# Optimization experiments

Hardware: AMD Instinct MI355X
Metric: run time of the kernel (lower is better)

The kernel has to match this reference:

```python
import jax, jax.numpy as jnp
import numpy as np

H = 256      # hidden_dim
NH = 8       # num_heads
D = H // NH  # per-head dim
NEG = -(2.0**32) + 1.0
EPS = 1e-5


def setup_inputs() -> dict:
    key = jax.random.key(0)
    ks = jax.random.split(key, 12)
    N, Tq, Tk = 2, 2048, 2048
    s = 1.0 / np.sqrt(H)
    return {
        "Q": jax.random.normal(ks[0], (N, Tq, H), jnp.float32),
        "K": jax.random.normal(ks[1], (N, Tk, H), jnp.float32),
        "V": jax.random.normal(ks[2], (N, Tk, H), jnp.float32),
        "Wq": jax.random.normal(ks[3], (H, H), jnp.float32) * s,
        "bq": jnp.zeros((H,), jnp.float32),
        "Wk": jax.random.normal(ks[4], (H, H), jnp.float32) * s,
        "bk": jnp.zeros((H,), jnp.float32),
        "Wv": jax.random.normal(ks[5], (H, H), jnp.float32) * s,
        "bv": jnp.zeros((H,), jnp.float32),
        "gamma": jnp.ones((H,), jnp.float32),
        "beta": jnp.zeros((H,), jnp.float32),
    }


def _split_heads(x):
    # [N,T,H] -> [h,N,T,D]  (matches torch split(dim=2)+cat(dim=0): head-major)
    N, T, _ = x.shape
    return x.reshape(N, T, NH, D).transpose(2, 0, 1, 3)


def reference(Q, K, V, Wq, bq, Wk, bk, Wv, bv, gamma, beta):
    N, Tq, _ = Q.shape
    Tk = K.shape[1]
    Ql = jax.nn.relu(Q @ Wq + bq)
    Kl = jax.nn.relu(K @ Wk + bk)
    Vl = jax.nn.relu(V @ Wv + bv)
    Qh, Kh, Vh = _split_heads(Ql), _split_heads(Kl), _split_heads(Vl)

    scores = jnp.einsum("hnqd,hnkd->hnqk", Qh, Kh) / jnp.sqrt(jnp.float32(D))
    key_mask = jnp.sign(jnp.abs(K).sum(-1))    # [N,Tk]
    scores = jnp.where(key_mask[None, :, None, :] == 0, NEG, scores)
    attn = jax.nn.softmax(scores / 0.01, axis=-1)
    query_mask = jnp.sign(jnp.abs(Q).sum(-1))  # [N,Tq]
    attn = attn * query_mask[None, :, :, None]  # dropout p=0 -> identity

    ctx = jnp.einsum("hnqk,hnkd->hnqd", attn[..., :-1], Vh[:, :, :-1, :])
    out = ctx.transpose(1, 2, 0, 3).reshape(N, Tq, H)

    mu = out.mean(-1, keepdims=True)
    var = ((out - mu) ** 2).mean(-1, keepdims=True)
    out = (out - mu) / jnp.sqrt(var + EPS) * gamma + beta

    weight = attn.transpose(1, 2, 0, 3).reshape(N, Tq, NH * Tk).mean(-1)
    return out, weight
```

## Files before the change

### kernel.cpp

```cpp
#include <hip/hip_runtime.h>
#include <math.h>

#define H_DIM 256
#define NHEAD 8
#define DHEAD 32
#define NB 2
#define TSEQ 2048
#define LN_EPS 1e-5f

#define QK2_SCALE 25.503486f
#define SPLIT 2
#define TILES_PER (TSEQ / 64 / SPLIT)

typedef _Float16 half8 __attribute__((ext_vector_type(8)));
typedef _Float16 half4t __attribute__((ext_vector_type(4)));
typedef _Float16 half2t __attribute__((ext_vector_type(2)));
typedef float f32x4 __attribute__((ext_vector_type(4)));

__device__ __forceinline__ f32x4 mfma16(half8 a, half8 b, f32x4 c) {
  return __builtin_amdgcn_mfma_f32_16x16x32_f16(a, b, c, 0, 0, 0);
}
__device__ __forceinline__ float exp2fast(float x) {
  return __builtin_amdgcn_exp2f(x);
}
__device__ __forceinline__ half2t pkrtz(float a, float b) {
  return __builtin_bit_cast(half2t, __builtin_amdgcn_cvt_pkrtz(a, b));
}

__global__ __launch_bounds__(256) void pack_mask_kernel(
    const float* __restrict__ K,
    const float* __restrict__ Wq, const float* __restrict__ Wk, const float* __restrict__ Wv,
    float* __restrict__ kmask,
    half8* __restrict__ WpkHi, half8* __restrict__ WpkLo) {
  const int tid = threadIdx.x;
  if (blockIdx.x < 1024) {
    const int wid = tid >> 6, lane = tid & 63;
    int row = blockIdx.x * 4 + wid;
    const float* src = K + (size_t)row * H_DIM;
    float4 v = *(const float4*)(src + lane * 4);
    float s = fabsf(v.x) + fabsf(v.y) + fabsf(v.z) + fabsf(v.w);
    #pragma unroll
    for (int off = 32; off > 0; off >>= 1) s += __shfl_xor(s, off);
    if (lane == 0) kmask[row] = (s != 0.0f) ? 1.0f : 0.0f;
    return;
  }
  int slot = (blockIdx.x - 1024) * 256 + tid;
  int lane = slot & 63;
  int fg = (slot >> 6) & 15;
  int s  = (slot >> 10) & 7;
  int which = slot >> 13;
  const float* W = which == 0 ? Wq : which == 1 ? Wk : Wv;
  int j  = fg * 16 + (lane & 15);
  int kb = s * 32 + (lane >> 4) * 8;
  half8 hi, lo;
  #pragma unroll
  for (int jj = 0; jj < 8; ++jj) {
    float x = W[(size_t)(kb + jj) * H_DIM + j];
    _Float16 h = (_Float16)x;
    hi[jj] = h;
    lo[jj] = (_Float16)(x - (float)h);
  }
  WpkHi[slot] = hi;
  WpkLo[slot] = lo;
}

__global__ __launch_bounds__(256) void proj_kernel(
    const float* __restrict__ Q, const float* __restrict__ K, const float* __restrict__ V,
    const float* __restrict__ bq, const float* __restrict__ bk, const float* __restrict__ bv,
    const half8* __restrict__ WpkHi, const half8* __restrict__ WpkLo,
    const float* __restrict__ kmask,
    half8* __restrict__ Gqhi, half8* __restrict__ Gqlo,
    half8* __restrict__ Gkhi, half8* __restrict__ Gklo, half8* __restrict__ Gv,
    half8* __restrict__ AmaskF, float* __restrict__ qmask) {
  const int which = blockIdx.z;
  const float* X    = which == 0 ? Q  : which == 1 ? K  : V;
  const float* bias = which == 0 ? bq : which == 1 ? bk : bv;

  __shared__ __align__(16) float T[64 * 68];

  const int tid = threadIdx.x;
  const int w = tid >> 6, lane = tid & 63;
  const int l15 = lane & 15, quad = lane >> 4;
  const int mbase = blockIdx.y * 64;
  const int nfg   = blockIdx.x * 4;
  const int nn   = mbase >> 11;
  const int tile = blockIdx.y & 31;

  half8 ahi[8], alo[8];
  {
    const bool doqm = (which == 0) && (blockIdx.x == 0);
    float sabs = 0.0f;
    const float* xrow = X + (size_t)(mbase + w * 16 + l15) * H_DIM + quad * 8;
    #pragma unroll
    for (int s = 0; s < 8; ++s) {
      float4 a0 = *(const float4*)(xrow + s * 32);
      float4 a1 = *(const float4*)(xrow + s * 32 + 4);
      float xs[8] = {a0.x, a0.y, a0.z, a0.w, a1.x, a1.y, a1.z, a1.w};
      if (doqm) {
        #pragma unroll
        for (int i = 0; i < 8; ++i) sabs += fabsf(xs[i]);
      }
      #pragma unroll
      for (int i = 0; i < 8; ++i) {
        _Float16 h = (_Float16)xs[i];
        ahi[s][i] = h;
        alo[s][i] = (_Float16)(xs[i] - (float)h);
      }
    }
    if (doqm) {
      sabs += __shfl_xor(sabs, 16);
      sabs += __shfl_xor(sabs, 32);
      if (quad == 0) qmask[mbase + w * 16 + l15] = (sabs != 0.0f) ? 1.0f : 0.0f;
    }
  }

  f32x4 acc[4];
  #pragma unroll
  for (int f = 0; f < 4; ++f) acc[f] = (f32x4){0.f, 0.f, 0.f, 0.f};

  #pragma unroll
  for (int s = 0; s < 8; ++s) {
    const half8* ph = WpkHi + (((size_t)which * 8 + s) * 16 + nfg) * 64 + lane;
    const half8* pl = WpkLo + (((size_t)which * 8 + s) * 16 + nfg) * 64 + lane;
    #pragma unroll
    for (int f = 0; f < 4; ++f) {
      half8 BH = ph[f * 64];
      half8 BL = pl[f * 64];
      acc[f] = mfma16(ahi[s], BH, acc[f]);
      acc[f] = mfma16(ahi[s], BL, acc[f]);
      acc[f] = mfma16(alo[s], BH, acc[f]);
    }
  }

  #pragma unroll
  for (int f = 0; f < 4; ++f) {
    float bj = bias[blockIdx.x * 64 + f * 16 + l15];
    #pragma unroll
    for (int r = 0; r < 4; ++r) {
      int row = w * 16 + quad * 4 + r;
      float val = fmaxf(acc[f][r] + bj, 0.0f);
      if (which == 2 && ((mbase + row) & (TSEQ - 1)) == TSEQ - 1) val = 0.0f;
      T[row * 68 + f * 16 + l15] = val;
    }
  }
  __syncthreads();

  if (which < 2) {
    const int fq = tid >> 6, lp = tid & 63;
    const int kdc = lp >> 4, krlo = lp & 15;
    const int row = fq * 16 + krlo;
    const float sc = (which == 0) ? QK2_SCALE : 1.0f;
    #pragma unroll
    for (int hs = 0; hs < 2; ++hs) {
      const float* p = &T[row * 68 + hs * 32 + kdc * 8];
      float4 a0 = *(const float4*)p;
      float4 a1 = *(const float4*)(p + 4);
      float xs[8] = {a0.x, a0.y, a0.z, a0.w, a1.x, a1.y, a1.z, a1.w};
      half8 hi, lo;
      #pragma unroll
      for (int i = 0; i < 8; ++i) {
        float x = xs[i] * sc;
        _Float16 h = (_Float16)x;
        hi[i] = h;
        lo[i] = (_Float16)(x - (float)h);
      }
      int hn = (blockIdx.x * 2 + hs) * NB + nn;
      size_t di = ((size_t)hn * 32 + tile) * 256 + tid;
      if (which == 0) { Gqhi[di] = hi; Gqlo[di] = lo; }
      else            { Gkhi[di] = hi; Gklo[di] = lo; }
    }
    if (which == 1 && blockIdx.x == 0 && tid < 128) {
      int c = tid >> 6, lane2 = tid & 63;
      int quad2 = lane2 >> 4, l15b = lane2 & 15;
      half8 am;
      #pragma unroll
      for (int j = 0; j < 8; ++j)
        am[j] = (l15b == 0) ? (_Float16)kmask[(size_t)nn * TSEQ + tile * 64 + c * 32 + quad2 * 8 + j]
                            : (_Float16)0.0f;
      AmaskF[(((size_t)nn * 32 + tile) * 2 + c) * 64 + lane2] = am;
    }
  } else {
    const int top = tid >> 6, mid = (tid >> 4) & 3, low = tid & 15;
    const int c = top >> 1, hh = top & 1;
    const int trow0 = (c * 4 + mid) * 8;
    float km[8];
    #pragma unroll
    for (int j = 0; j < 8; ++j)
      km[j] = kmask[(size_t)nn * TSEQ + tile * 64 + trow0 + j];
    #pragma unroll
    for (int hs = 0; hs < 2; ++hs) {
      const int col = hs * 32 + hh * 16 + low;
      half8 v8;
      #pragma unroll
      for (int j = 0; j < 8; ++j)
        v8[j] = (_Float16)(T[(trow0 + j) * 68 + col] * km[j]);
      int hn = (blockIdx.x * 2 + hs) * NB + nn;
      Gv[((size_t)hn * 32 + tile) * 256 + tid] = v8;
    }
  }
}

__global__ __launch_bounds__(256, 4) void attn_kernel(
    const half8* __restrict__ Gqhi, const half8* __restrict__ Gqlo,
    const half8* __restrict__ Gkhi, const half8* __restrict__ Gklo,
    const half8* __restrict__ Gv, const half8* __restrict__ AmaskF,
    _Float16* __restrict__ Opf, float* __restrict__ Mp, float* __restrict__ Lp) {
  __shared__ __align__(16) half8 KhB[2][256];
  __shared__ __align__(16) half8 KlB[2][256];
  __shared__ __align__(16) half8 VB[2][256];
  __shared__ __align__(16) half8 AB[2][128];
  __shared__ __align__(16) _Float16 Pbuf[4][16][72];

  const int tid = threadIdx.x;
  const int w = tid >> 6, lane = tid & 63;
  const int l15 = lane & 15, quad = lane >> 4;

  const int b = blockIdx.x;
  const int g    = ((b & 7) << 1) | ((b >> 3) & 1);
  const int qt   = (b >> 4) & 31;
  const int sblk = b >> 9;
  const int n = g & 1;

  const size_t fbase = (size_t)g * 32 * 256;
  const int tile0 = sblk * TILES_PER;

  half8 qhi = Gqhi[fbase + (size_t)qt * 256 + w * 64 + lane];
  half8 qlo = Gqlo[fbase + (size_t)qt * 256 + w * 64 + lane];

  float m_q = -1.0e30f;
  f32x4 O0, O1, Ol;
  O0 = (f32x4){0.f, 0.f, 0.f, 0.f};
  O1 = (f32x4){0.f, 0.f, 0.f, 0.f};
  Ol = (f32x4){0.f, 0.f, 0.f, 0.f};

  const half8* gkh = Gkhi + fbase + (size_t)tile0 * 256;
  const half8* gkl = Gklo + fbase + (size_t)tile0 * 256;
  const half8* gvv = Gv   + fbase + (size_t)tile0 * 256;
  const half8* gam = AmaskF + (size_t)(n * 32 + tile0) * 128;

  KhB[0][tid] = gkh[tid];
  KlB[0][tid] = gkl[tid];
  VB[0][tid]  = gvv[tid];
  if (tid < 128) AB[0][tid] = gam[tid];
  __syncthreads();

  #pragma unroll
  for (int tt = 0; tt < TILES_PER; ++tt) {
    const int cur = tt & 1, nxt = cur ^ 1;
    half8 rkh, rkl, rv, ra;
    if (tt < TILES_PER - 1) {
      rkh = gkh[(tt + 1) * 256 + tid];
      rkl = gkl[(tt + 1) * 256 + tid];
      rv  = gvv[(tt + 1) * 256 + tid];
      if (tid < 128) ra = gam[(tt + 1) * 128 + tid];
    }

    f32x4 S[4];
    #pragma unroll
    for (int f = 0; f < 4; ++f) {
      half8 KH = KhB[cur][f * 64 + lane];
      half8 KL = KlB[cur][f * 64 + lane];
      f32x4 a = (f32x4){0.f, 0.f, 0.f, 0.f};
      a = mfma16(KL, qhi, a);
      a = mfma16(KH, qlo, a);
      a = mfma16(KH, qhi, a);
      S[f] = a;
    }

    float t0 = fmaxf(fmaxf(S[0][0], S[0][1]), fmaxf(S[0][2], S[0][3]));
    float t1 = fmaxf(fmaxf(S[1][0], S[1][1]), fmaxf(S[1][2], S[1][3]));
    float t2 = fmaxf(fmaxf(S[2][0], S[2][1]), fmaxf(S[2][2], S[2][3]));
    float t3 = fmaxf(fmaxf(S[3][0], S[3][1]), fmaxf(S[3][2], S[3][3]));
    float mx = fmaxf(fmaxf(t0, t1), fmaxf(t2, t3));
    mx = fmaxf(mx, __shfl_xor(mx, 16));
    mx = fmaxf(mx, __shfl_xor(mx, 32));

    float mnew = fmaxf(m_q, mx);
    float alpha = exp2fast(m_q - mnew);
    m_q = mnew;

    #pragma unroll
    for (int f = 0; f < 4; ++f) {
      float p0 = exp2fast(S[f][0] - m_q);
      float p1 = exp2fast(S[f][1] - m_q);
      float p2 = exp2fast(S[f][2] - m_q);
      float p3 = exp2fast(S[f][3] - m_q);
      half2t a01 = pkrtz(p0, p1);
      half2t a23 = pkrtz(p2, p3);
      half4t pk4;
      pk4[0] = a01[0]; pk4[1] = a01[1]; pk4[2] = a23[0]; pk4[3] = a23[1];
      *(half4t*)&Pbuf[w][l15][f * 16 + quad * 4] = pk4;
    }
    #pragma unroll
    for (int r = 0; r < 4; ++r) { O0[r] *= alpha; O1[r] *= alpha; }
    Ol[0] *= alpha;
    asm volatile("s_waitcnt lgkmcnt(0)" ::: "memory");

    half8 am0 = AB[cur][lane];
    half8 am1 = AB[cur][64 + lane];
    const half8* vbuf = (const half8*)VB[cur];
    #pragma unroll
    for (int c = 0; c < 2; ++c) {
      half8 pb = *(const half8*)&Pbuf[w][l15][c * 32 + quad * 8];
      O0 = mfma16(vbuf[(c * 2 + 0) * 64 + lane], pb, O0);
      O1 = mfma16(vbuf[(c * 2 + 1) * 64 + lane], pb, O1);
      Ol = mfma16(c == 0 ? am0 : am1, pb, Ol);
    }

    if (tt < TILES_PER - 1) {
      KhB[nxt][tid] = rkh;
      KlB[nxt][tid] = rkl;
      VB[nxt][tid]  = rv;
      if (tid < 128) AB[nxt][tid] = ra;
    }
    __syncthreads();
  }

  {
    int q = qt * 64 + w * 16 + l15;
    size_t idx = ((size_t)(sblk * 16 + g) * TSEQ + q) * DHEAD;
    half4t o0 = {(_Float16)O0[0], (_Float16)O0[1], (_Float16)O0[2], (_Float16)O0[3]};
    half4t o1 = {(_Float16)O1[0], (_Float16)O1[1], (_Float16)O1[2], (_Float16)O1[3]};
    *(half4t*)&Opf[idx + quad * 4]      = o0;
    *(half4t*)&Opf[idx + 16 + quad * 4] = o1;
    if (quad == 0) {
      Mp[(size_t)(sblk * 16 + g) * TSEQ + q] = m_q;
      Lp[(size_t)(sblk * 16 + g) * TSEQ + q] = Ol[0];
    }
  }
}

__global__ __launch_bounds__(256) void ln_kernel(
    const _Float16* __restrict__ Opf, const float* __restrict__ Mp, const float* __restrict__ Lp,
    const float* __restrict__ gamma, const float* __restrict__ beta,
    const float* __restrict__ qmask,
    float* __restrict__ out, float* __restrict__ wout) {
  const int wid = threadIdx.x >> 6, lane = threadIdx.x & 63;
  const int row = blockIdx.x * 4 + wid;
  const int n = row >> 11, q = row & (TSEQ - 1);
  const int hh = lane >> 3;
  const int hn = hh * NB + n;
  const int dbase = (lane & 7) * 4;

  float m[SPLIT], l[SPLIT];
  half4t P[SPLIT];
  #pragma unroll
  for (int i = 0; i < SPLIT; ++i) {
    size_t si = (size_t)(i * 16 + hn) * TSEQ + q;
    P[i] = *(const half4t*)&Opf[si * DHEAD + dbase];
    m[i] = Mp[si];
    l[i] = Lp[si];
  }
  float mm = m[0];
  #pragma unroll
  for (int i = 1; i < SPLIT; ++i) mm = fmaxf(mm, m[i]);
  float denom = 0.f;
  float a[SPLIT];
  #pragma unroll
  for (int i = 0; i < SPLIT; ++i) { a[i] = exp2fast(m[i] - mm); denom += l[i] * a[i]; }
  float qm = qmask[row];
  float inv = qm / denom;

  float4 x = make_float4(0.f, 0.f, 0.f, 0.f);
  #pragma unroll
  for (int i = 0; i < SPLIT; ++i) {
    x.x += (float)P[i][0] * a[i]; x.y += (float)P[i][1] * a[i];
    x.z += (float)P[i][2] * a[i]; x.w += (float)P[i][3] * a[i];
  }
  x.x *= inv; x.y *= inv; x.z *= inv; x.w *= inv;

  float s = x.x + x.y + x.z + x.w;
  #pragma unroll
  for (int off = 32; off > 0; off >>= 1) s += __shfl_xor(s, off);
  float mu = s * (1.0f / H_DIM);
  float dx0 = x.x - mu, dx1 = x.y - mu, dx2 = x.z - mu, dx3 = x.w - mu;
  float sq = dx0 * dx0 + dx1 * dx1 + dx2 * dx2 + dx3 * dx3;
  #pragma unroll
  for (int off = 32; off > 0; off >>= 1) sq += __shfl_xor(sq, off);
  float rstd = rsqrtf(sq * (1.0f / H_DIM) + LN_EPS);
  float4 g = *(const float4*)(gamma + lane * 4);
  float4 bb = *(const float4*)(beta + lane * 4);
  float4 y;
  y.x = dx0 * rstd * g.x + bb.x;
  y.y = dx1 * rstd * g.y + bb.y;
  y.z = dx2 * rstd * g.z + bb.z;
  y.w = dx3 * rstd * g.w + bb.w;
  *(float4*)(out + (size_t)row * H_DIM + lane * 4) = y;
  if (lane == 0) wout[row] = qm * (1.0f / TSEQ);
}

extern "C" void kernel_launch(void* const* d_in, const int* in_sizes, int n_in,
                              void* d_out, int out_size, void* d_ws, size_t ws_size,
                              hipStream_t stream) {
  const float* Q  = (const float*)d_in[0];
  const float* K  = (const float*)d_in[1];
  const float* V  = (const float*)d_in[2];
  const float* Wq = (const float*)d_in[3];
  const float* bq = (const float*)d_in[4];
  const float* Wk = (const float*)d_in[5];
  const float* bk = (const float*)d_in[6];
  const float* Wv = (const float*)d_in[7];
  const float* bv = (const float*)d_in[8];
  const float* gamma = (const float*)d_in[9];
  const float* beta  = (const float*)d_in[10];

  char* ws = (char*)d_ws;
  const size_t NFRAG = (size_t)16 * 32 * 256;
  _Float16* Opf = (_Float16*)ws;
  half8* Gqhi = (half8*)(ws + (size_t)SPLIT * 16 * TSEQ * DHEAD * 2);
  half8* Gqlo = Gqhi + NFRAG;
  half8* Gkhi = Gqlo + NFRAG;
  half8* Gklo = Gkhi + NFRAG;
  half8* Gv   = Gklo + NFRAG;
  float* Mp = (float*)(Gv + NFRAG);
  float* Lp = Mp + SPLIT * 16 * TSEQ;
  float* qmask = Lp + SPLIT * 16 * TSEQ;
  float* kmask = qmask + NB * TSEQ;
  half8* WpkHi = (half8*)(kmask + NB * TSEQ);
  half8* WpkLo = WpkHi + 24576;
  half8* AmaskF = WpkLo + 24576;

  float* out  = (float*)d_out;
  float* wout = out + (size_t)NB * TSEQ * H_DIM;

  hipLaunchKernelGGL(pack_mask_kernel, dim3(1024 + 96), dim3(256), 0, stream,
                     K, Wq, Wk, Wv, kmask, WpkHi, WpkLo);
  hipLaunchKernelGGL(proj_kernel, dim3(H_DIM / 64, NB * TSEQ / 64, 3), dim3(256), 0, stream,
                     Q, K, V, bq, bk, bv, WpkHi, WpkLo, kmask,
                     Gqhi, Gqlo, Gkhi, Gklo, Gv, AmaskF, qmask);
  hipLaunchKernelGGL(attn_kernel, dim3(16 * 32 * SPLIT), dim3(256), 0, stream,
                     Gqhi, Gqlo, Gkhi, Gklo, Gv, AmaskF, Opf, Mp, Lp);
  hipLaunchKernelGGL(ln_kernel, dim3(NB * TSEQ / 4), dim3(256), 0, stream,
                     Opf, Mp, Lp, gamma, beta, qmask, out, wout);
}
```

Measured before the change: 127.3 us.

## Process two query tiles per block, double KV split, load K/V directly to LDS

Each attention block now handles two 64-row query tiles and reuses every K/V tile it loads for both, which halves K/V traffic per query. The KV split goes from 2 to 4 so the grid keeps the same block count. K/V/mask prefetch uses global_load_lds to write straight into shared memory, skipping the register staging and the explicit LDS stores. proj_kernel also gets a launch-bounds occupancy hint. In exchange, register pressure in the attention kernel goes up and the LN kernel has more partials to merge; the async LDS loads rely on __syncthreads for ordering.

```diff
diff --git a/kernel.cpp b/kernel.cpp
--- a/kernel.cpp
+++ b/kernel.cpp
@@ -9,7 +9,7 @@
 #define LN_EPS 1e-5f
 
 #define QK2_SCALE 25.503486f
-#define SPLIT 2
+#define SPLIT 4
 #define TILES_PER (TSEQ / 64 / SPLIT)
 
 typedef _Float16 half8 __attribute__((ext_vector_type(8)));
@@ -26,6 +26,11 @@
 __device__ __forceinline__ half2t pkrtz(float a, float b) {
   return __builtin_bit_cast(half2t, __builtin_amdgcn_cvt_pkrtz(a, b));
 }
+
+#define GLOAD_LDS(gp, lp)                                            \
+  __builtin_amdgcn_global_load_lds(                                  \
+      (const __attribute__((address_space(1))) void*)(gp),           \
+      (__attribute__((address_space(3))) void*)(lp), 16, 0, 0)
 
 __global__ __launch_bounds__(256) void pack_mask_kernel(
     const float* __restrict__ K,
@@ -64,7 +69,7 @@
   WpkLo[slot] = lo;
 }
 
-__global__ __launch_bounds__(256) void proj_kernel(
+__global__ __launch_bounds__(256, 3) void proj_kernel(
     const float* __restrict__ Q, const float* __restrict__ K, const float* __restrict__ V,
     const float* __restrict__ bq, const float* __restrict__ bk, const float* __restrict__ bv,
     const half8* __restrict__ WpkHi, const half8* __restrict__ WpkLo,
@@ -217,115 +222,127 @@
 
   const int b = blockIdx.x;
   const int g    = ((b & 7) << 1) | ((b >> 3) & 1);
-  const int qt   = (b >> 4) & 31;
-  const int sblk = b >> 9;
+  const int qt   = (b >> 4) & 15;
+  const int sblk = b >> 8;
   const int n = g & 1;
 
   const size_t fbase = (size_t)g * 32 * 256;
   const int tile0 = sblk * TILES_PER;
 
-  half8 qhi = Gqhi[fbase + (size_t)qt * 256 + w * 64 + lane];
-  half8 qlo = Gqlo[fbase + (size_t)qt * 256 + w * 64 + lane];
-
-  float m_q = -1.0e30f;
-  f32x4 O0, O1, Ol;
-  O0 = (f32x4){0.f, 0.f, 0.f, 0.f};
-  O1 = (f32x4){0.f, 0.f, 0.f, 0.f};
-  Ol = (f32x4){0.f, 0.f, 0.f, 0.f};
+  const size_t qoff = fbase + (size_t)(qt * 2) * 256 + w * 64 + lane;
+  half8 qhiA = Gqhi[qoff];
+  half8 qloA = Gqlo[qoff];
+  half8 qhiB = Gqhi[qoff + 256];
+  half8 qloB = Gqlo[qoff + 256];
+
+  float mA = -1.0e30f, mB = -1.0e30f;
+  f32x4 O0A = {0.f,0.f,0.f,0.f}, O1A = O0A, OlA = O0A;
+  f32x4 O0B = O0A, O1B = O0A, OlB = O0A;
 
   const half8* gkh = Gkhi + fbase + (size_t)tile0 * 256;
   const half8* gkl = Gklo + fbase + (size_t)tile0 * 256;
   const half8* gvv = Gv   + fbase + (size_t)tile0 * 256;
   const half8* gam = AmaskF + (size_t)(n * 32 + tile0) * 128;
 
-  KhB[0][tid] = gkh[tid];
-  KlB[0][tid] = gkl[tid];
-  VB[0][tid]  = gvv[tid];
-  if (tid < 128) AB[0][tid] = gam[tid];
+  GLOAD_LDS(gkh + tid, &KhB[0][tid]);
+  GLOAD_LDS(gkl + tid, &KlB[0][tid]);
+  GLOAD_LDS(gvv + tid, &VB[0][tid]);
+  if (tid < 128) GLOAD_LDS(gam + tid, &AB[0][tid]);
   __syncthreads();
 
   #pragma unroll
   for (int tt = 0; tt < TILES_PER; ++tt) {
     const int cur = tt & 1, nxt = cur ^ 1;
-    half8 rkh, rkl, rv, ra;
     if (tt < TILES_PER - 1) {
-      rkh = gkh[(tt + 1) * 256 + tid];
-      rkl = gkl[(tt + 1) * 256 + tid];
-      rv  = gvv[(tt + 1) * 256 + tid];
-      if (tid < 128) ra = gam[(tt + 1) * 128 + tid];
-    }
-
-    f32x4 S[4];
+      GLOAD_LDS(gkh + (tt + 1) * 256 + tid, &KhB[nxt][tid]);
+      GLOAD_LDS(gkl + (tt + 1) * 256 + tid, &KlB[nxt][tid]);
+      GLOAD_LDS(gvv + (tt + 1) * 256 + tid, &VB[nxt][tid]);
+      if (tid < 128) GLOAD_LDS(gam + (tt + 1) * 128 + tid, &AB[nxt][tid]);
+    }
+
+    f32x4 SA[4], SB[4];
     #pragma unroll
     for (int f = 0; f < 4; ++f) {
       half8 KH = KhB[cur][f * 64 + lane];
       half8 KL = KlB[cur][f * 64 + lane];
       f32x4 a = (f32x4){0.f, 0.f, 0.f, 0.f};
-      a = mfma16(KL, qhi, a);
-      a = mfma16(KH, qlo, a);
-      a = mfma16(KH, qhi, a);
-      S[f] = a;
-    }
-
-    float t0 = fmaxf(fmaxf(S[0][0], S[0][1]), fmaxf(S[0][2], S[0][3]));
-    float t1 = fmaxf(fmaxf(S[1][0], S[1][1]), fmaxf(S[1][2], S[1][3]));
-    float t2 = fmaxf(fmaxf(S[2][0], S[2][1]), fmaxf(S[2][2], S[2][3]));
-    float t3 = fmaxf(fmaxf(S[3][0], S[3][1]), fmaxf(S[3][2], S[3][3]));
-    float mx = fmaxf(fmaxf(t0, t1), fmaxf(t2, t3));
-    mx = fmaxf(mx, __shfl_xor(mx, 16));
-    mx = fmaxf(mx, __shfl_xor(mx, 32));
-
-    float mnew = fmaxf(m_q, mx);
-    float alpha = exp2fast(m_q - mnew);
-    m_q = mnew;
-
-    #pragma unroll
-    for (int f = 0; f < 4; ++f) {
-      float p0 = exp2fast(S[f][0] - m_q);
-      float p1 = exp2fast(S[f][1] - m_q);
-      float p2 = exp2fast(S[f][2] - m_q);
-      float p3 = exp2fast(S[f][3] - m_q);
-      half2t a01 = pkrtz(p0, p1);
-      half2t a23 = pkrtz(p2, p3);
-      half4t pk4;
-      pk4[0] = a01[0]; pk4[1] = a01[1]; pk4[2] = a23[0]; pk4[3] = a23[1];
-      *(half4t*)&Pbuf[w][l15][f * 16 + quad * 4] = pk4;
-    }
-    #pragma unroll
-    for (int r = 0; r < 4; ++r) { O0[r] *= alpha; O1[r] *= alpha; }
-    Ol[0] *= alpha;
-    asm volatile("s_waitcnt lgkmcnt(0)" ::: "memory");
+      a = mfma16(KL, qhiA, a);
+      a = mfma16(KH, qloA, a);
+      a = mfma16(KH, qhiA, a);
+      SA[f] = a;
+      f32x4 bb = (f32x4){0.f, 0.f, 0.f, 0.f};
+      bb = mfma16(KL, qhiB, bb);
+      bb = mfma16(KH, qloB, bb);
+      bb = mfma16(KH, qhiB, bb);
+      SB[f] = bb;
+    }
 
     half8 am0 = AB[cur][lane];
     half8 am1 = AB[cur][64 + lane];
     const half8* vbuf = (const half8*)VB[cur];
-    #pragma unroll
-    for (int c = 0; c < 2; ++c) {
-      half8 pb = *(const half8*)&Pbuf[w][l15][c * 32 + quad * 8];
-      O0 = mfma16(vbuf[(c * 2 + 0) * 64 + lane], pb, O0);
-      O1 = mfma16(vbuf[(c * 2 + 1) * 64 + lane], pb, O1);
-      Ol = mfma16(c == 0 ? am0 : am1, pb, Ol);
-    }
-
-    if (tt < TILES_PER - 1) {
-      KhB[nxt][tid] = rkh;
-      KlB[nxt][tid] = rkl;
-      VB[nxt][tid]  = rv;
-      if (tid < 128) AB[nxt][tid] = ra;
-    }
+
+#define SM_PV(S, m_q, O0, O1, Ol)                                              \
+    {                                                                          \
+      float t0 = fmaxf(fmaxf(S[0][0], S[0][1]), fmaxf(S[0][2], S[0][3]));      \
+      float t1 = fmaxf(fmaxf(S[1][0], S[1][1]), fmaxf(S[1][2], S[1][3]));      \
+      float t2 = fmaxf(fmaxf(S[2][0], S[2][1]), fmaxf(S[2][2], S[2][3]));      \
+      float t3 = fmaxf(fmaxf(S[3][0], S[3][1]), fmaxf(S[3][2], S[3][3]));      \
+      float mx = fmaxf(fmaxf(t0, t1), fmaxf(t2, t3));                          \
+      mx = fmaxf(mx, __shfl_xor(mx, 16));                                      \
+      mx = fmaxf(mx, __shfl_xor(mx, 32));                                      \
+      float mnew = fmaxf(m_q, mx);                                             \
+      float alpha = exp2fast(m_q - mnew);                                      \
+      m_q = mnew;                                                              \
+      _Pragma("unroll")                                                        \
+      for (int f = 0; f < 4; ++f) {                                            \
+        float p0 = exp2fast(S[f][0] - m_q);                                    \
+        float p1 = exp2fast(S[f][1] - m_q);                                    \
+        float p2 = exp2fast(S[f][2] - m_q);                                    \
+        float p3 = exp2fast(S[f][3] - m_q);                                    \
+        half2t a01 = pkrtz(p0, p1);                                            \
+        half2t a23 = pkrtz(p2, p3);                                            \
+        half4t pk4;                                                            \
+        pk4[0] = a01[0]; pk4[1] = a01[1]; pk4[2] = a23[0]; pk4[3] = a23[1];    \
+        *(half4t*)&Pbuf[w][l15][f * 16 + quad * 4] = pk4;                      \
+      }                                                                        \
+      _Pragma("unroll")                                                        \
+      for (int r = 0; r < 4; ++r) { O0[r] *= alpha; O1[r] *= alpha; }          \
+      Ol[0] *= alpha;                                                          \
+      asm volatile("s_waitcnt lgkmcnt(0)" ::: "memory");                       \
+      _Pragma("unroll")                                                        \
+      for (int c = 0; c < 2; ++c) {                                            \
+        half8 pb = *(const half8*)&Pbuf[w][l15][c * 32 + quad * 8];            \
+        O0 = mfma16(vbuf[(c * 2 + 0) * 64 + lane], pb, O0);                    \
+        O1 = mfma16(vbuf[(c * 2 + 1) * 64 + lane], pb, O1);                    \
+        Ol = mfma16(c == 0 ? am0 : am1, pb, Ol);                               \
+      }                                                                        \
+    }
+
+    SM_PV(SA, mA, O0A, O1A, OlA)
+    SM_PV(SB, mB, O0B, O1B, OlB)
+#undef SM_PV
+
     __syncthreads();
   }
 
   {
-    int q = qt * 64 + w * 16 + l15;
-    size_t idx = ((size_t)(sblk * 16 + g) * TSEQ + q) * DHEAD;
-    half4t o0 = {(_Float16)O0[0], (_Float16)O0[1], (_Float16)O0[2], (_Float16)O0[3]};
-    half4t o1 = {(_Float16)O1[0], (_Float16)O1[1], (_Float16)O1[2], (_Float16)O1[3]};
-    *(half4t*)&Opf[idx + quad * 4]      = o0;
-    *(half4t*)&Opf[idx + 16 + quad * 4] = o1;
+    int qA = qt * 128 + w * 16 + l15;
+    size_t rowbase = (size_t)(sblk * 16 + g) * TSEQ;
+    size_t idxA = (rowbase + qA) * DHEAD;
+    size_t idxB = (rowbase + qA + 64) * DHEAD;
+    half4t o0A = {(_Float16)O0A[0], (_Float16)O0A[1], (_Float16)O0A[2], (_Float16)O0A[3]};
+    half4t o1A = {(_Float16)O1A[0], (_Float16)O1A[1], (_Float16)O1A[2], (_Float16)O1A[3]};
+    half4t o0B = {(_Float16)O0B[0], (_Float16)O0B[1], (_Float16)O0B[2], (_Float16)O0B[3]};
+    half4t o1B = {(_Float16)O1B[0], (_Float16)O1B[1], (_Float16)O1B[2], (_Float16)O1B[3]};
+    *(half4t*)&Opf[idxA + quad * 4]      = o0A;
+    *(half4t*)&Opf[idxA + 16 + quad * 4] = o1A;
+    *(half4t*)&Opf[idxB + quad * 4]      = o0B;
+    *(half4t*)&Opf[idxB + 16 + quad * 4] = o1B;
     if (quad == 0) {
-      Mp[(size_t)(sblk * 16 + g) * TSEQ + q] = m_q;
-      Lp[(size_t)(sblk * 16 + g) * TSEQ + q] = Ol[0];
+      Mp[rowbase + qA]      = mA;
+      Lp[rowbase + qA]      = OlA[0];
+      Mp[rowbase + qA + 64] = mB;
+      Lp[rowbase + qA + 64] = OlB[0];
     }
   }
 }
@@ -428,7 +445,7 @@
   hipLaunchKernelGGL(proj_kernel, dim3(H_DIM / 64, NB * TSEQ / 64, 3), dim3(256), 0, stream,
                      Q, K, V, bq, bk, bv, WpkHi, WpkLo, kmask,
                      Gqhi, Gqlo, Gkhi, Gklo, Gv, AmaskF, qmask);
-  hipLaunchKernelGGL(attn_kernel, dim3(16 * 32 * SPLIT), dim3(256), 0, stream,
+  hipLaunchKernelGGL(attn_kernel, dim3(16 * 16 * SPLIT), dim3(256), 0, stream,
                      Gqhi, Gqlo, Gkhi, Gklo, Gv, AmaskF, Opf, Mp, Lp);
   hipLaunchKernelGGL(ln_kernel, dim3(NB * TSEQ / 4), dim3(256), 0, stream,
                      Opf, Mp, Lp, gamma, beta, qmask, out, wout);
```

New measurement: 124.4 us. -2.3%, faster.
